# Performance work log

Measured on AMD Instinct MI355X. Metric: run time of the kernel, lower is better.

The kernel has to match this reference:

```python
import jax, jax.numpy as jnp
import numpy as np

N, L, V, H = 64, 2048, 32000, 512

def setup_inputs() -> dict:
    key = jax.random.key(0)
    ks = jax.random.split(key, 6)
    s = 1.0 / np.sqrt(H)
    return {
        "X": jax.random.randint(ks[0], (N, L), 0, V),
        "emb": jax.random.normal(ks[1], (V, H), jnp.float32),
        "W_hh": jax.random.normal(ks[2], (H, H), jnp.float32) * s,
        "b_hh": jax.random.normal(ks[3], (H,), jnp.float32) * s,
        "W_xh": jax.random.normal(ks[4], (H, H), jnp.float32) * s,
        "b_xh": jax.random.normal(ks[5], (H,), jnp.float32) * s,
    }

def reference(X, emb, W_hh, b_hh, W_xh, b_xh):
    # Embed all timesteps and apply the input projection once (batched GEMM);
    # identical math to per-step W_xh(E_t) + b_xh.
    E = emb[X]                                   # (N, L, H)
    Xh = jnp.einsum('nlh,kh->nlk', E, W_xh) + b_xh  # (N, L, H)

    def step(h, xh_t):
        # h_t = tanh(W_hh h_{t-1} + b_hh + W_xh x_t + b_xh)
        h = jnp.tanh(h @ W_hh.T + b_hh + xh_t)
        return h, h

    h0 = jnp.zeros((X.shape[0], W_hh.shape[0]), dtype=emb.dtype)
    _, H_all = jax.lax.scan(step, h0, jnp.swapaxes(Xh, 0, 1))  # (L, N, H)
    return jnp.swapaxes(H_all, 0, 1)             # (N, L, H)
```

## Files before the change

kernel.cpp:

```cpp
#include <hip/hip_runtime.h>


typedef _Float16 half8 __attribute__((ext_vector_type(8)));
typedef float    f32x4 __attribute__((ext_vector_type(4)));

#define MFMA_F16(A,B,C) __builtin_amdgcn_mfma_f32_16x16x32_f16(A,B,C,0,0,0)

static __device__ __forceinline__ half8 cvt8(const float* p){
  const f32x4* q = (const f32x4*)p;
  f32x4 a = q[0], b = q[1];
  half8 r;
  r[0]=(_Float16)a[0]; r[1]=(_Float16)a[1]; r[2]=(_Float16)a[2]; r[3]=(_Float16)a[3];
  r[4]=(_Float16)b[0]; r[5]=(_Float16)b[1]; r[6]=(_Float16)b[2]; r[7]=(_Float16)b[3];
  return r;
}

static __device__ __forceinline__ float tanh_fast(float z){
  float e = __expf(2.0f*z);
  return 1.0f - 2.0f/(e + 1.0f);
}

__global__ __launch_bounds__(256) void k_xh(
    const int* __restrict__ X, const float* __restrict__ emb,
    const float* __restrict__ Wxh, const float* __restrict__ bxh,
    const float* __restrict__ bhh, float* __restrict__ out)
{
  const int bid = blockIdx.x;
  const int bm = bid >> 3;
  const int bn = bid & 7;
  const int tid = threadIdx.x;
  const int w  = tid >> 6;
  const int l  = tid & 63;
  const int lr = l & 15, lq = l >> 4;

  const int mbase = bm*64 + (w>>1)*32;
  const int nbase = bn*64 + (w&1)*32;

  const int tok0 = X[mbase + lr];
  const int tok1 = X[mbase + 16 + lr];
  const int c0 = nbase + lr;
  const int c1 = nbase + 16 + lr;
  const float bs0 = bxh[c0] + bhh[c0];
  const float bs1 = bxh[c1] + bhh[c1];

  const float* a0 = emb + (long long)tok0*512 + lq*8;
  const float* a1 = emb + (long long)tok1*512 + lq*8;
  const float* b0 = Wxh + (long long)c0*512 + lq*8;
  const float* b1 = Wxh + (long long)c1*512 + lq*8;

  f32x4 acc00 = {0,0,0,0}, acc01 = {0,0,0,0}, acc10 = {0,0,0,0}, acc11 = {0,0,0,0};

  #pragma unroll
  for (int ks=0; ks<16; ++ks){
    half8 A0 = cvt8(a0 + ks*32);
    half8 A1 = cvt8(a1 + ks*32);
    half8 B0 = cvt8(b0 + ks*32);
    half8 B1 = cvt8(b1 + ks*32);
    acc00 = MFMA_F16(A0, B0, acc00);
    acc01 = MFMA_F16(A0, B1, acc01);
    acc10 = MFMA_F16(A1, B0, acc10);
    acc11 = MFMA_F16(A1, B1, acc11);
  }
  #pragma unroll
  for (int r=0; r<4; ++r){
    const long long m0 = mbase + 4*lq + r;
    const long long m1 = m0 + 16;
    out[m0*512 + c0] = acc00[r] + bs0;
    out[m0*512 + c1] = acc01[r] + bs1;
    out[m1*512 + c0] = acc10[r] + bs0;
    out[m1*512 + c1] = acc11[r] + bs1;
  }
}

__global__ __launch_bounds__(256, 1) void k_rnn(
    const float* __restrict__ Whh,
    float* __restrict__ out)
{
  const int g   = blockIdx.x;
  const int tid = threadIdx.x;
  const int w   = tid >> 6;
  const int l   = tid & 63;
  const int lr  = l & 15;
  const int kg  = l >> 4;
  const int r7  = lr & 7;
  const int colbase = w * 128;

  __shared__ _Float16 wlds[4][32][512];
  __shared__ _Float16 hb[16][512];

  {
    f32x4 z = {0,0,0,0};
    f32x4* hz = (f32x4*)&hb[0][0];
    for (int i = tid; i < 16*512*2/16; i += 256) hz[i] = z;
  }

  half8 Wreg[8][12];
  #pragma unroll
  for (int ct = 0; ct < 8; ++ct){
    const float* wp = Whh + (long long)(colbase + ct*16 + lr)*512 + kg*8;
    #pragma unroll
    for (int ks = 0; ks < 16; ++ks){
      half8 v = cvt8(wp + ks*32);
      if ((ks & 3) == 0) *(half8*)&wlds[w][ct*4 + (ks>>2)][l*8] = v;
      else               Wreg[ct][ks - (ks>>2) - 1] = v;
    }
  }
  __syncthreads();

  const long long nbase = (long long)(g*16 + lr) * (2048LL*512);

  for (int t = 0; t < 2048; ++t){
    const float* op = out + nbase + (long long)t*512 + colbase + kg*4;
    f32x4 xh[8];
    #pragma unroll
    for (int ct = 0; ct < 8; ++ct) xh[ct] = *(const f32x4*)(op + ct*16);

    f32x4 acc[8];
    #pragma unroll
    for (int ct = 0; ct < 8; ++ct) acc[ct] = (f32x4){0,0,0,0};

    #pragma unroll
    for (int ks = 0; ks < 16; ++ks){
      half8 hf = *(const half8*)((const char*)&hb[lr][0] + (((4*ks + kg) ^ r7) << 4));
      if ((ks & 3) == 0){
        const int fs = ks >> 2;
        #pragma unroll
        for (int ct = 0; ct < 8; ++ct)
          acc[ct] = MFMA_F16(*(const half8*)&wlds[w][ct*4 + fs][l*8], hf, acc[ct]);
      } else {
        const int j = ks - (ks>>2) - 1;
        #pragma unroll
        for (int ct = 0; ct < 8; ++ct)
          acc[ct] = MFMA_F16(Wreg[ct][j], hf, acc[ct]);
      }
    }
    __syncthreads();

    #pragma unroll
    for (int ct = 0; ct < 8; ++ct){
      f32x4 hv;
      #pragma unroll
      for (int r = 0; r < 4; ++r) hv[r] = tanh_fast(acc[ct][r] + xh[ct][r]);
      *(f32x4*)(out + nbase + (long long)t*512 + colbase + ct*16 + kg*4) = hv;

      union { _Float16 h[4]; unsigned long long u; } pk;
      #pragma unroll
      for (int r = 0; r < 4; ++r) pk.h[r] = (_Float16)hv[r];
      const int byte = (colbase + ct*16 + kg*4) * 2;
      const int c0   = byte >> 4;
      const int off8 = byte & 15;
      *(unsigned long long*)((char*)&hb[lr][0] + (((c0 ^ r7) << 4) + off8)) = pk.u;
    }
    __syncthreads();
  }
}

extern "C" void kernel_launch(void* const* d_in, const int* in_sizes, int n_in,
                              void* d_out, int out_size, void* d_ws, size_t ws_size,
                              hipStream_t stream)
{
  const int*   X    = (const int*)  d_in[0];
  const float* emb  = (const float*)d_in[1];
  const float* Whh  = (const float*)d_in[2];
  const float* bhh  = (const float*)d_in[3];
  const float* Wxh  = (const float*)d_in[4];
  const float* bxh  = (const float*)d_in[5];
  float* out = (float*)d_out;

  hipLaunchKernelGGL(k_xh,  dim3(16384), dim3(256), 0, stream, X, emb, Wxh, bxh, bhh, out);
  hipLaunchKernelGGL(k_rnn, dim3(4),     dim3(256), 0, stream, Whh, out);
}
```

Before: 9.969 ms.

## Keep half of W_hh resident in AGPRs and feed MFMA directly from them

Repartitions the register-resident recurrent weights: half of the W_hh fragments are pinned in accumulation registers (AGPRs) via inline asm and used directly as MFMA A operands, a quarter stay in VGPRs, and only a quarter come from LDS. Previously a quarter lived in LDS and three quarters in VGPRs. The aim is to cut per-step LDS traffic and VGPR pressure in the serial recurrence loop by using the otherwise idle AGPR file. It risks compiler spills or extra accumulate-register moves, and the volatile asm may limit scheduling.

```diff
diff --git a/kernel.cpp b/kernel.cpp
--- a/kernel.cpp
+++ b/kernel.cpp
@@ -5,6 +5,11 @@
 typedef float    f32x4 __attribute__((ext_vector_type(4)));
 
 #define MFMA_F16(A,B,C) __builtin_amdgcn_mfma_f32_16x16x32_f16(A,B,C,0,0,0)
+
+static __device__ __forceinline__ void mfma_agpr(f32x4& acc, half8 w, half8 h){
+  asm volatile("v_mfma_f32_16x16x32_f16 %0, %1, %2, %0"
+               : "+v"(acc) : "a"(w), "v"(h));
+}
 
 static __device__ __forceinline__ half8 cvt8(const float* p){
   const f32x4* q = (const f32x4*)p;
@@ -83,7 +88,7 @@
   const int lr  = l & 15;
   const int kg  = l >> 4;
   const int r7  = lr & 7;
-  const int colbase = w * 128;
+  const int colb = 128*w;
 
   __shared__ _Float16 wlds[4][32][512];
   __shared__ _Float16 hb[16][512];
@@ -91,26 +96,28 @@
   {
     f32x4 z = {0,0,0,0};
     f32x4* hz = (f32x4*)&hb[0][0];
-    for (int i = tid; i < 16*512*2/16; i += 256) hz[i] = z;
+    for (int i = tid; i < 1024; i += 256) hz[i] = z;
   }
 
-  half8 Wreg[8][12];
+  half8 Wa[64], Wv[32];
   #pragma unroll
   for (int ct = 0; ct < 8; ++ct){
-    const float* wp = Whh + (long long)(colbase + ct*16 + lr)*512 + kg*8;
+    const float* wp = Whh + (long long)(colb + ct*16 + lr)*512 + kg*8;
     #pragma unroll
     for (int ks = 0; ks < 16; ++ks){
       half8 v = cvt8(wp + ks*32);
-      if ((ks & 3) == 0) *(half8*)&wlds[w][ct*4 + (ks>>2)][l*8] = v;
-      else               Wreg[ct][ks - (ks>>2) - 1] = v;
+      const int f = ct*16 + ks;
+      if ((f & 1) == 0){ asm("" : "+a"(v)); Wa[f>>1] = v; }
+      else if ((f & 3) == 1){ Wv[f>>2] = v; }
+      else { *(half8*)&wlds[w][f>>2][l*8] = v; }
     }
   }
   __syncthreads();
 
-  const long long nbase = (long long)(g*16 + lr) * (2048LL*512);
+  const long long nb = (long long)(g*16 + lr) * (2048LL*512);
 
   for (int t = 0; t < 2048; ++t){
-    const float* op = out + nbase + (long long)t*512 + colbase + kg*4;
+    const float* op = out + nb + (long long)t*512 + colb + kg*4;
     f32x4 xh[8];
     #pragma unroll
     for (int ct = 0; ct < 8; ++ct) xh[ct] = *(const f32x4*)(op + ct*16);
@@ -119,19 +126,19 @@
     #pragma unroll
     for (int ct = 0; ct < 8; ++ct) acc[ct] = (f32x4){0,0,0,0};
 
+    const char* hrow = (const char*)&hb[lr][0];
     #pragma unroll
     for (int ks = 0; ks < 16; ++ks){
-      half8 hf = *(const half8*)((const char*)&hb[lr][0] + (((4*ks + kg) ^ r7) << 4));
-      if ((ks & 3) == 0){
-        const int fs = ks >> 2;
-        #pragma unroll
-        for (int ct = 0; ct < 8; ++ct)
-          acc[ct] = MFMA_F16(*(const half8*)&wlds[w][ct*4 + fs][l*8], hf, acc[ct]);
-      } else {
-        const int j = ks - (ks>>2) - 1;
-        #pragma unroll
-        for (int ct = 0; ct < 8; ++ct)
-          acc[ct] = MFMA_F16(Wreg[ct][j], hf, acc[ct]);
+      half8 hf = *(const half8*)(hrow + (((4*ks + kg) ^ r7) << 4));
+      #pragma unroll
+      for (int ct = 0; ct < 8; ++ct){
+        const int f = ct*16 + ks;
+        if ((f & 1) == 0)       mfma_agpr(acc[ct], Wa[f>>1], hf);
+        else if ((f & 3) == 1)  acc[ct] = MFMA_F16(Wv[f>>2], hf, acc[ct]);
+        else {
+          half8 wl = *(const half8*)&wlds[w][f>>2][l*8];
+          acc[ct] = MFMA_F16(wl, hf, acc[ct]);
+        }
       }
     }
     __syncthreads();
@@ -141,15 +148,14 @@
       f32x4 hv;
       #pragma unroll
       for (int r = 0; r < 4; ++r) hv[r] = tanh_fast(acc[ct][r] + xh[ct][r]);
-      *(f32x4*)(out + nbase + (long long)t*512 + colbase + ct*16 + kg*4) = hv;
+      *(f32x4*)(op + ct*16) = hv;
 
       union { _Float16 h[4]; unsigned long long u; } pk;
       #pragma unroll
       for (int r = 0; r < 4; ++r) pk.h[r] = (_Float16)hv[r];
-      const int byte = (colbase + ct*16 + kg*4) * 2;
-      const int c0   = byte >> 4;
-      const int off8 = byte & 15;
-      *(unsigned long long*)((char*)&hb[lr][0] + (((c0 ^ r7) << 4) + off8)) = pk.u;
+      const int byte = (colb + ct*16 + kg*4) * 2;
+      char* wrow = (char*)&hb[lr][0];
+      *(unsigned long long*)(wrow + ((((byte >> 4) ^ r7) << 4) + (byte & 15))) = pk.u;
     }
     __syncthreads();
   }
```

New measurement: 11.67 ms. 1.17x slower.
